# Optimization experiments

Measured on AMD Instinct MI355X. Metric: run time of the kernel, lower is better.

The kernel has to match this reference:

```python
import jax, jax.numpy as jnp
import numpy as np

D_MODEL = 1024
D_FF = 4096
LN_EPS = 1e-5


def _layer_norm(x, gamma, beta):
    mu = jnp.mean(x, axis=-1, keepdims=True)
    var = jnp.mean(jnp.square(x - mu), axis=-1, keepdims=True)
    return (x - mu) * jax.lax.rsqrt(var + LN_EPS) * gamma + beta


def setup_inputs() -> dict:
    key = jax.random.key(0)
    ks = jax.random.split(key, 16)
    B, S, D, F = 2, 2048, D_MODEL, D_FF
    s_d = 1.0 / np.sqrt(D)
    s_f = 1.0 / np.sqrt(F)
    u = lambda k, shape, s: jax.random.uniform(k, shape, jnp.float32, -s, s)
    return {
        "x": jax.random.normal(ks[0], (B, S, D), jnp.float32),
        "wq": u(ks[1], (D, D), s_d), "bq": u(ks[2], (D,), s_d),
        "wk": u(ks[3], (D, D), s_d), "bk": u(ks[4], (D,), s_d),
        "wv": u(ks[5], (D, D), s_d), "bv": u(ks[6], (D,), s_d),
        "wo": u(ks[7], (D, D), s_d), "bo": u(ks[8], (D,), s_d),
        "w1": u(ks[9], (F, D), s_d), "b1": u(ks[10], (F,), s_d),
        "w2": u(ks[11], (D, F), s_f), "b2": u(ks[12], (D,), s_f),
        "g1": jnp.ones((D,), jnp.float32), "be1": jnp.zeros((D,), jnp.float32),
        "g2": jnp.ones((D,), jnp.float32), "be2": jnp.zeros((D,), jnp.float32),
        "num_heads": 16,
    }


def reference(x, wq, bq, wk, bk, wv, bv, wo, bo, w1, b1, w2, b2, g1, be1, g2, be2, num_heads):
    B, S, D = x.shape
    H = num_heads
    dk = D // H
    scale = 1.0 / np.sqrt(dk)

    # --- self-attention (pre-norm) ---
    h = _layer_norm(x, g1, be1)
    q = (h @ wq.T + bq).reshape(B, S, H, dk)
    k = (h @ wk.T + bk).reshape(B, S, H, dk)
    v = (h @ wv.T + bv).reshape(B, S, H, dk)
    scores = jnp.einsum("bqhd,bkhd->bhqk", q, k) * scale  # [B,H,S,S]
    attn = jax.nn.softmax(scores, axis=-1)
    ctx = jnp.einsum("bhqk,bkhd->bqhd", attn, v).reshape(B, S, D)
    x = x + ctx @ wo.T + bo

    # --- feed-forward (pre-norm, exact GELU as in torch default) ---
    h = _layer_norm(x, g2, be2)
    h = jax.nn.gelu(h @ w1.T + b1, approximate=False)
    x = x + h @ w2.T + b2
    return x
```

## Files before the change

kernel.cpp:

```cpp
#include <hip/hip_runtime.h>

typedef __attribute__((ext_vector_type(8))) __bf16 bf16x8;
typedef __attribute__((ext_vector_type(4))) __bf16 bf16x4;
typedef __attribute__((ext_vector_type(4))) float floatx4;
typedef void __attribute__((address_space(3))) lds_void_t;
typedef const void __attribute__((address_space(1))) gbl_void_t;

#define D_MODEL 1024
#define SEQ     2048
#define BATCH   2
#define NH      16
#define DK      64
#define DFF     4096
#define NTOK    (BATCH * SEQ)
#define QKVS    3072

#if __has_builtin(__builtin_amdgcn_exp2f)
#define EXP2(x) __builtin_amdgcn_exp2f(x)
#else
#define EXP2(x) exp2f(x)
#endif

__device__ __forceinline__ float gelu_exact(float x) {
    return 0.5f * x * (1.0f + erff(x * 0.70710678118654752f));
}

__global__ __launch_bounds__(256) void cast_f32_bf16(const float* __restrict__ src,
                                                     __bf16* __restrict__ dst, int n) {
    int i = (blockIdx.x * 256 + threadIdx.x) * 8;
    if (i >= n) return;
    floatx4 a = *(const floatx4*)(src + i);
    floatx4 b = *(const floatx4*)(src + i + 4);
    bf16x8 o;
    for (int j = 0; j < 4; ++j) { o[j] = (__bf16)a[j]; o[4 + j] = (__bf16)b[j]; }
    *(bf16x8*)(dst + i) = o;
}

__global__ __launch_bounds__(64) void ln_kernel(const float* __restrict__ x,
                                                const float* __restrict__ g,
                                                const float* __restrict__ b,
                                                __bf16* __restrict__ out) {
    int row = blockIdx.x, lane = threadIdx.x, base = lane * 16;
    const float* xr = x + (size_t)row * D_MODEL + base;
    float v[16];
    for (int j = 0; j < 4; ++j) {
        floatx4 a = *(const floatx4*)(xr + 4 * j);
        for (int i = 0; i < 4; ++i) v[4 * j + i] = a[i];
    }
    float s = 0.f, sq = 0.f;
    for (int i = 0; i < 16; ++i) { s += v[i]; sq += v[i] * v[i]; }
    for (int o = 1; o < 64; o <<= 1) { s += __shfl_xor(s, o); sq += __shfl_xor(sq, o); }
    float mu = s * (1.0f / D_MODEL);
    float var = sq * (1.0f / D_MODEL) - mu * mu;
    float rstd = rsqrtf(fmaxf(var, 0.f) + 1e-5f);

    const floatx4* gp = (const floatx4*)(g + base);
    const floatx4* bp = (const floatx4*)(b + base);
    bf16x8 o0, o1;
    for (int j = 0; j < 2; ++j) {
        floatx4 gv0 = gp[2 * j], gv1 = gp[2 * j + 1];
        floatx4 bv0 = bp[2 * j], bv1 = bp[2 * j + 1];
        for (int i = 0; i < 4; ++i) {
            float r0 = (v[8 * j + i] - mu) * rstd * gv0[i] + bv0[i];
            float r1 = (v[8 * j + 4 + i] - mu) * rstd * gv1[i] + bv1[i];
            if (j == 0) { o0[i] = (__bf16)r0; o0[4 + i] = (__bf16)r1; }
            else        { o1[i] = (__bf16)r0; o1[4 + i] = (__bf16)r1; }
        }
    }
    bf16x8* op = (bf16x8*)(out + (size_t)row * D_MODEL + base);
    op[0] = o0; op[1] = o1;
}

template <typename OutT, bool GELU, bool TRIBIAS, int KSPLIT>
__global__ __launch_bounds__(256) void gemm_bt(const __bf16* __restrict__ A,
                                               const __bf16* __restrict__ W,
                                               const float* __restrict__ bias0,
                                               const float* __restrict__ bias1,
                                               const float* __restrict__ bias2,
                                               const float* __restrict__ res,
                                               OutT* out, float* part1,
                                               int M, int N, int K) {
    __shared__ __bf16 As[2][128][32];
    __shared__ __bf16 Ws[2][128][32];

    int m0 = blockIdx.y * 128, n0 = blockIdx.x * 128;
    int t = threadIdx.x;
    int lane = t & 63, wave = t >> 6;
    int wm = (wave >> 1) * 64, wn = (wave & 1) * 64;
    int fr = lane & 15, quad = lane >> 4;
    int srow = t >> 2, scol = (t & 3) * 8;

    int Ks = K / KSPLIT;
    int kbeg = (KSPLIT > 1) ? blockIdx.z * Ks : 0;

    floatx4 acc[4][4] = {};

    const __bf16* Ab = A + (size_t)(m0 + srow) * K + kbeg + scol;
    const __bf16* Wb = W + (size_t)(n0 + srow) * K + kbeg + scol;

    auto stage = [&](int buf, int k0) {
        __builtin_amdgcn_global_load_lds((gbl_void_t*)(Ab + k0),
                                         (lds_void_t*)&As[buf][wave * 16][0], 16, 0, 0);
        __builtin_amdgcn_global_load_lds((gbl_void_t*)(Ab + (size_t)64 * K + k0),
                                         (lds_void_t*)&As[buf][64 + wave * 16][0], 16, 0, 0);
        __builtin_amdgcn_global_load_lds((gbl_void_t*)(Wb + k0),
                                         (lds_void_t*)&Ws[buf][wave * 16][0], 16, 0, 0);
        __builtin_amdgcn_global_load_lds((gbl_void_t*)(Wb + (size_t)64 * K + k0),
                                         (lds_void_t*)&Ws[buf][64 + wave * 16][0], 16, 0, 0);
    };

    stage(0, 0);
    int nsteps = Ks / 32;
    for (int s = 0; s < nsteps; ++s) {
        int cur = s & 1;
        __syncthreads();
        if (s + 1 < nsteps) stage(cur ^ 1, (s + 1) * 32);

        bf16x8 af[4], wf[4];
#pragma unroll
        for (int i = 0; i < 4; ++i) af[i] = *(const bf16x8*)&As[cur][wm + i * 16 + fr][quad * 8];
#pragma unroll
        for (int i = 0; i < 4; ++i) wf[i] = *(const bf16x8*)&Ws[cur][wn + i * 16 + fr][quad * 8];
#pragma unroll
        for (int mi = 0; mi < 4; ++mi)
#pragma unroll
            for (int ni = 0; ni < 4; ++ni)
                acc[mi][ni] = __builtin_amdgcn_mfma_f32_16x16x32_bf16(af[mi], wf[ni], acc[mi][ni], 0, 0, 0);
    }

    if (KSPLIT > 1) {
        float* pb = (blockIdx.z == 0) ? (float*)out : part1;
#pragma unroll
        for (int ni = 0; ni < 4; ++ni) {
            int col = n0 + wn + ni * 16 + fr;
#pragma unroll
            for (int mi = 0; mi < 4; ++mi)
#pragma unroll
                for (int r = 0; r < 4; ++r) {
                    int row = m0 + wm + mi * 16 + quad * 4 + r;
                    pb[(size_t)row * N + col] = acc[mi][ni][r];
                }
        }
    } else {
#pragma unroll
        for (int ni = 0; ni < 4; ++ni) {
            int col = n0 + wn + ni * 16 + fr;
            const float* bp = bias0;
            int bcol = col;
            if (TRIBIAS) { bp = col < 1024 ? bias0 : (col < 2048 ? bias1 : bias2); bcol = col & 1023; }
            float bv = bp[bcol];
#pragma unroll
            for (int mi = 0; mi < 4; ++mi) {
#pragma unroll
                for (int r = 0; r < 4; ++r) {
                    int row = m0 + wm + mi * 16 + quad * 4 + r;
                    float v = acc[mi][ni][r] + bv;
                    if (GELU) v = gelu_exact(v);
                    if (res) v += res[(size_t)row * N + col];
                    out[(size_t)row * N + col] = (OutT)v;
                }
            }
        }
    }
}

__global__ __launch_bounds__(256) void reduce_k2(const float* __restrict__ p0,
                                                 const float* p1,
                                                 const float* __restrict__ res,
                                                 const float* __restrict__ bias,
                                                 float* out) {
    int i = (blockIdx.x * 256 + threadIdx.x) * 4;
    floatx4 a = *(const floatx4*)(p0 + i);
    floatx4 b = *(const floatx4*)(p1 + i);
    floatx4 r = *(const floatx4*)(res + i);
    floatx4 bv = *(const floatx4*)(bias + (i & 1023));
    floatx4 o;
#pragma unroll
    for (int j = 0; j < 4; ++j) o[j] = a[j] + b[j] + r[j] + bv[j];
    *(floatx4*)(out + i) = o;
}

__global__ __launch_bounds__(256) void transpose_v(const __bf16* __restrict__ qkv,
                                                   __bf16* __restrict__ vt) {
    __shared__ __bf16 tile[64][72];
    int b = blockIdx.z, h = blockIdx.y, s0 = blockIdx.x * 64;
    int t = threadIdx.x;
    int dl = (t & 7) * 8, sl = t >> 3;
    for (int p = 0; p < 2; ++p) {
        int s = sl + p * 32;
        bf16x8 val = *(const bf16x8*)(qkv + (size_t)(b * SEQ + s0 + s) * QKVS + 2048 + h * DK + dl);
        *(bf16x8*)&tile[s][dl] = val;
    }
    __syncthreads();
    int sl2 = (t & 7) * 8, d = t >> 3;
    for (int p = 0; p < 2; ++p) {
        int dd = d + p * 32;
        bf16x8 val;
        for (int j = 0; j < 8; ++j) val[j] = tile[sl2 + j][dd];
        *(bf16x8*)(vt + ((size_t)(b * NH + h) * DK + dd) * SEQ + s0 + sl2) = val;
    }
}

__global__ __launch_bounds__(256, 2) void attn_kernel(const __bf16* __restrict__ qkv,
                                                      const __bf16* __restrict__ vt,
                                                      __bf16* __restrict__ ctx) {
    __shared__ __bf16 Klds[8192];
    __shared__ __bf16 Vlds[8192];
    __shared__ __bf16 Plds[4][32][136];
    int b = blockIdx.z, h = blockIdx.y;
    int wave = threadIdx.x >> 6, lane = threadIdx.x & 63;
    int q0 = blockIdx.x * 128 + wave * 32;
    int fr = lane & 15, quad = lane >> 4;
    const float sc2 = 0.18033688011112042f;

    const __bf16* qp0 = qkv + (size_t)(b * SEQ + q0 + fr) * QKVS + h * DK + quad * 8;
    const __bf16* qp1 = qp0 + (size_t)16 * QKVS;
    bf16x8 qA0 = *(const bf16x8*)qp0, qB0 = *(const bf16x8*)(qp0 + 32);
    bf16x8 qA1 = *(const bf16x8*)qp1, qB1 = *(const bf16x8*)(qp1 + 32);

    const __bf16* kg = qkv + (size_t)b * SEQ * QKVS + 1024 + h * DK;
    const __bf16* vg = vt + (size_t)(b * NH + h) * DK * SEQ;

    floatx4 o[8] = {};
    float m0q = -1e30f, l0q = 0.f, m1q = -1e30f, l1q = 0.f;

    auto stage_tile = [&](int k0) {
#pragma unroll
        for (int p = 0; p < 4; ++p) {
            int bid = wave * 4 + p;
            int f = bid >> 1, half = bid & 1;
            __builtin_amdgcn_global_load_lds(
                (gbl_void_t*)(kg + (size_t)(k0 + f * 16 + fr) * QKVS + quad * 8 + half * 32),
                (lds_void_t*)&Klds[bid * 512], 16, 0, 0);
            int c = bid >> 2, ti = bid & 3;
            __builtin_amdgcn_global_load_lds(
                (gbl_void_t*)(vg + (size_t)(ti * 16 + fr) * SEQ + k0 + c * 32 + quad * 8),
                (lds_void_t*)&Vlds[bid * 512], 16, 0, 0);
        }
    };

    stage_tile(0);
    __syncthreads();

    for (int k0 = 0; k0 < SEQ; k0 += 128) {
        const __bf16* Kb = Klds + lane * 8;
        const __bf16* Vb = Vlds + lane * 8;
        bf16x8 kA[8], kB[8];
#pragma unroll
        for (int f = 0; f < 8; ++f) {
            kA[f] = *(const bf16x8*)(Kb + (f * 2 + 0) * 512);
            kB[f] = *(const bf16x8*)(Kb + (f * 2 + 1) * 512);
        }

        floatx4 s[8];
#pragma unroll
        for (int f = 0; f < 8; ++f) {
            floatx4 z = {0.f, 0.f, 0.f, 0.f};
            z = __builtin_amdgcn_mfma_f32_16x16x32_bf16(kA[f], qA0, z, 0, 0, 0);
            s[f] = __builtin_amdgcn_mfma_f32_16x16x32_bf16(kB[f], qB0, z, 0, 0, 0);
        }
        {
            float fm[8];
#pragma unroll
            for (int f = 0; f < 8; ++f)
                fm[f] = fmaxf(fmaxf(s[f][0], s[f][1]), fmaxf(s[f][2], s[f][3]));
            float mx = fmaxf(fmaxf(fmaxf(fm[0], fm[1]), fmaxf(fm[2], fm[3])),
                             fmaxf(fmaxf(fm[4], fm[5]), fmaxf(fm[6], fm[7])));
            float mx2 = mx * sc2;
            mx2 = fmaxf(mx2, __shfl_xor(mx2, 16));
            mx2 = fmaxf(mx2, __shfl_xor(mx2, 32));
            float mn = fmaxf(m0q, mx2);
            float alpha = EXP2(m0q - mn);
            m0q = mn;
            float r0 = 0.f, r1 = 0.f, r2 = 0.f, r3 = 0.f;
#pragma unroll
            for (int f = 0; f < 8; ++f) {
                bf16x4 pk;
                float p0 = EXP2(fmaf(s[f][0], sc2, -mn));
                float p1 = EXP2(fmaf(s[f][1], sc2, -mn));
                float p2 = EXP2(fmaf(s[f][2], sc2, -mn));
                float p3 = EXP2(fmaf(s[f][3], sc2, -mn));
                r0 += p0; r1 += p1; r2 += p2; r3 += p3;
                pk[0] = (__bf16)p0; pk[1] = (__bf16)p1; pk[2] = (__bf16)p2; pk[3] = (__bf16)p3;
                *(bf16x4*)&Plds[wave][fr][f * 16 + quad * 4] = pk;
            }
            float rs = (r0 + r1) + (r2 + r3);
            rs += __shfl_xor(rs, 16);
            rs += __shfl_xor(rs, 32);
            l0q = l0q * alpha + rs;
            float aB[4];
#pragma unroll
            for (int r = 0; r < 4; ++r) aB[r] = __shfl(alpha, quad * 4 + r);
#pragma unroll
            for (int ti = 0; ti < 4; ++ti)
#pragma unroll
                for (int r = 0; r < 4; ++r) o[ti][r] *= aB[r];
        }

        floatx4 s1[8];
#pragma unroll
        for (int f = 0; f < 8; ++f) {
            floatx4 z = {0.f, 0.f, 0.f, 0.f};
            z = __builtin_amdgcn_mfma_f32_16x16x32_bf16(kA[f], qA1, z, 0, 0, 0);
            s1[f] = __builtin_amdgcn_mfma_f32_16x16x32_bf16(kB[f], qB1, z, 0, 0, 0);
        }

        bf16x8 vf[4][4];
#pragma unroll
        for (int c = 0; c < 4; ++c)
#pragma unroll
            for (int ti = 0; ti < 4; ++ti)
                vf[c][ti] = *(const bf16x8*)(Vb + (c * 4 + ti) * 512);

        __syncthreads();
        if (k0 + 128 < SEQ) stage_tile(k0 + 128);

        {
            float fm[8];
#pragma unroll
            for (int f = 0; f < 8; ++f)
                fm[f] = fmaxf(fmaxf(s1[f][0], s1[f][1]), fmaxf(s1[f][2], s1[f][3]));
            float mx = fmaxf(fmaxf(fmaxf(fm[0], fm[1]), fmaxf(fm[2], fm[3])),
                             fmaxf(fmaxf(fm[4], fm[5]), fmaxf(fm[6], fm[7])));
            float mx2 = mx * sc2;
            mx2 = fmaxf(mx2, __shfl_xor(mx2, 16));
            mx2 = fmaxf(mx2, __shfl_xor(mx2, 32));
            float mn = fmaxf(m1q, mx2);
            float alpha = EXP2(m1q - mn);
            m1q = mn;
            float r0 = 0.f, r1 = 0.f, r2 = 0.f, r3 = 0.f;
#pragma unroll
            for (int f = 0; f < 8; ++f) {
                bf16x4 pk;
                float p0 = EXP2(fmaf(s1[f][0], sc2, -mn));
                float p1 = EXP2(fmaf(s1[f][1], sc2, -mn));
                float p2 = EXP2(fmaf(s1[f][2], sc2, -mn));
                float p3 = EXP2(fmaf(s1[f][3], sc2, -mn));
                r0 += p0; r1 += p1; r2 += p2; r3 += p3;
                pk[0] = (__bf16)p0; pk[1] = (__bf16)p1; pk[2] = (__bf16)p2; pk[3] = (__bf16)p3;
                *(bf16x4*)&Plds[wave][16 + fr][f * 16 + quad * 4] = pk;
            }
            float rs = (r0 + r1) + (r2 + r3);
            rs += __shfl_xor(rs, 16);
            rs += __shfl_xor(rs, 32);
            l1q = l1q * alpha + rs;
            float aB[4];
#pragma unroll
            for (int r = 0; r < 4; ++r) aB[r] = __shfl(alpha, quad * 4 + r);
#pragma unroll
            for (int ti = 0; ti < 4; ++ti)
#pragma unroll
                for (int r = 0; r < 4; ++r) o[4 + ti][r] *= aB[r];
        }
        __threadfence_block();

        bf16x8 pa0[4], pa1[4];
#pragma unroll
        for (int c = 0; c < 4; ++c) {
            pa0[c] = *(const bf16x8*)&Plds[wave][fr][c * 32 + quad * 8];
            pa1[c] = *(const bf16x8*)&Plds[wave][16 + fr][c * 32 + quad * 8];
        }
#pragma unroll
        for (int c = 0; c < 4; ++c)
#pragma unroll
            for (int ti = 0; ti < 4; ++ti) {
                o[ti]     = __builtin_amdgcn_mfma_f32_16x16x32_bf16(pa0[c], vf[c][ti], o[ti], 0, 0, 0);
                o[4 + ti] = __builtin_amdgcn_mfma_f32_16x16x32_bf16(pa1[c], vf[c][ti], o[4 + ti], 0, 0, 0);
            }
        __threadfence_block();

        __syncthreads();
    }
    float lB0[4], lB1[4];
#pragma unroll
    for (int r = 0; r < 4; ++r) {
        lB0[r] = __shfl(l0q, quad * 4 + r);
        lB1[r] = __shfl(l1q, quad * 4 + r);
    }
#pragma unroll
    for (int ti = 0; ti < 4; ++ti)
#pragma unroll
        for (int r = 0; r < 4; ++r) {
            ctx[(size_t)(b * SEQ + q0 + quad * 4 + r) * D_MODEL + h * DK + ti * 16 + fr] =
                (__bf16)(o[ti][r] / lB0[r]);
            ctx[(size_t)(b * SEQ + q0 + 16 + quad * 4 + r) * D_MODEL + h * DK + ti * 16 + fr] =
                (__bf16)(o[4 + ti][r] / lB1[r]);
        }
}

extern "C" void kernel_launch(void* const* d_in, const int* in_sizes, int n_in,
                              void* d_out, int out_size, void* d_ws, size_t ws_size,
                              hipStream_t stream) {
    const float* x   = (const float*)d_in[0];
    const float* wq  = (const float*)d_in[1];
    const float* bq  = (const float*)d_in[2];
    const float* wk  = (const float*)d_in[3];
    const float* bk  = (const float*)d_in[4];
    const float* wv  = (const float*)d_in[5];
    const float* bv  = (const float*)d_in[6];
    const float* wo  = (const float*)d_in[7];
    const float* bo  = (const float*)d_in[8];
    const float* w1  = (const float*)d_in[9];
    const float* b1  = (const float*)d_in[10];
    const float* w2  = (const float*)d_in[11];
    const float* b2  = (const float*)d_in[12];
    const float* g1  = (const float*)d_in[13];
    const float* be1 = (const float*)d_in[14];
    const float* g2  = (const float*)d_in[15];
    const float* be2 = (const float*)d_in[16];
    float* out = (float*)d_out;

    char* ws = (char*)d_ws;
    const size_t MB = 1024 * 1024;
    __bf16* wqkvB = (__bf16*)(ws);
    __bf16* woB   = (__bf16*)(ws + 6 * MB);
    __bf16* w1B   = (__bf16*)(ws + 8 * MB);
    __bf16* w2B   = (__bf16*)(ws + 16 * MB);
    __bf16* h1    = (__bf16*)(ws + 24 * MB);
    float*  x1    = (float*)(ws + 24 * MB);
    __bf16* qkv   = (__bf16*)(ws + 40 * MB);
    __bf16* vt    = (__bf16*)(ws + 64 * MB);
    __bf16* ffh   = (__bf16*)(ws + 40 * MB);
    float*  pA0   = (float*)(ws + 40 * MB);
    float*  pA1   = (float*)(ws + 56 * MB);
    float*  pF0   = (float*)(ws);
    __bf16* ctx   = (__bf16*)d_out;
    __bf16* h2    = (__bf16*)d_out;

    const int NDD = D_MODEL * D_MODEL;
    const int NDF = D_MODEL * DFF;
    cast_f32_bf16<<<NDD / 2048, 256, 0, stream>>>(wq, wqkvB, NDD);
    cast_f32_bf16<<<NDD / 2048, 256, 0, stream>>>(wk, wqkvB + NDD, NDD);
    cast_f32_bf16<<<NDD / 2048, 256, 0, stream>>>(wv, wqkvB + 2 * NDD, NDD);
    cast_f32_bf16<<<NDD / 2048, 256, 0, stream>>>(wo, woB, NDD);
    cast_f32_bf16<<<NDF / 2048, 256, 0, stream>>>(w1, w1B, NDF);
    cast_f32_bf16<<<NDF / 2048, 256, 0, stream>>>(w2, w2B, NDF);

    dim3 gQKV(QKVS / 128, NTOK / 128);
    dim3 gDz(D_MODEL / 128, NTOK / 128, 2);
    dim3 gF(DFF / 128, NTOK / 128);
    dim3 gTr(SEQ / 64, NH, BATCH);
    dim3 gAttn(SEQ / 128, NH, BATCH);
    int gRed = NTOK * D_MODEL / (256 * 4);

    ln_kernel<<<NTOK, 64, 0, stream>>>(x, g1, be1, h1);
    gemm_bt<__bf16, false, true, 1><<<gQKV, 256, 0, stream>>>(h1, wqkvB, bq, bk, bv, nullptr, qkv, nullptr, NTOK, QKVS, D_MODEL);
    transpose_v<<<gTr, 256, 0, stream>>>(qkv, vt);
    attn_kernel<<<gAttn, 256, 0, stream>>>(qkv, vt, ctx);
    gemm_bt<float, false, false, 2><<<gDz, 256, 0, stream>>>(ctx, woB, nullptr, nullptr, nullptr, nullptr, pA0, pA1, NTOK, D_MODEL, D_MODEL);
    reduce_k2<<<gRed, 256, 0, stream>>>(pA0, pA1, x, bo, x1);
    ln_kernel<<<NTOK, 64, 0, stream>>>(x1, g2, be2, h2);
    gemm_bt<__bf16, true, false, 1><<<gF, 256, 0, stream>>>(h2, w1B, b1, b1, b1, nullptr, ffh, nullptr, NTOK, DFF, D_MODEL);
    gemm_bt<float, false, false, 2><<<gDz, 256, 0, stream>>>(ffh, w2B, nullptr, nullptr, nullptr, nullptr, pF0, (float*)d_out, NTOK, D_MODEL, DFF);
    reduce_k2<<<gRed, 256, 0, stream>>>(pF0, (float*)d_out, x1, b2, out);
}
```

Before: 417.7 us.

## Triple-buffer GEMM LDS tiles with fragment-ordered layout and partial vmcnt waits

Replaces the double-buffered GEMM mainloop with a three-stage LDS ring that keeps two K-tiles in flight, using explicit s_waitcnt vmcnt(4) and raw barriers instead of __syncthreads. The LDS tiles are also stored in MFMA fragment order so each lane reads a contiguous 16-byte chunk, which removes strided LDS reads and bank conflicts. The goal is to hide global load latency behind MFMA work. The cost is more LDS per block, which may lower occupancy, and fragile hand-set wait counts.

```diff
diff --git a/kernel.cpp b/kernel.cpp
--- a/kernel.cpp
+++ b/kernel.cpp
@@ -80,53 +80,72 @@
                                                const float* __restrict__ res,
                                                OutT* out, float* part1,
                                                int M, int N, int K) {
-    __shared__ __bf16 As[2][128][32];
-    __shared__ __bf16 Ws[2][128][32];
+    __shared__ __bf16 AsF[3][4096];
+    __shared__ __bf16 WsF[3][4096];
 
     int m0 = blockIdx.y * 128, n0 = blockIdx.x * 128;
     int t = threadIdx.x;
     int lane = t & 63, wave = t >> 6;
     int wm = (wave >> 1) * 64, wn = (wave & 1) * 64;
     int fr = lane & 15, quad = lane >> 4;
-    int srow = t >> 2, scol = (t & 3) * 8;
+    int scol = quad * 8;
 
     int Ks = K / KSPLIT;
     int kbeg = (KSPLIT > 1) ? blockIdx.z * Ks : 0;
 
     floatx4 acc[4][4] = {};
 
-    const __bf16* Ab = A + (size_t)(m0 + srow) * K + kbeg + scol;
-    const __bf16* Wb = W + (size_t)(n0 + srow) * K + kbeg + scol;
+    const __bf16* Abase = A + kbeg;
+    const __bf16* Wbase = W + kbeg;
 
     auto stage = [&](int buf, int k0) {
-        __builtin_amdgcn_global_load_lds((gbl_void_t*)(Ab + k0),
-                                         (lds_void_t*)&As[buf][wave * 16][0], 16, 0, 0);
-        __builtin_amdgcn_global_load_lds((gbl_void_t*)(Ab + (size_t)64 * K + k0),
-                                         (lds_void_t*)&As[buf][64 + wave * 16][0], 16, 0, 0);
-        __builtin_amdgcn_global_load_lds((gbl_void_t*)(Wb + k0),
-                                         (lds_void_t*)&Ws[buf][wave * 16][0], 16, 0, 0);
-        __builtin_amdgcn_global_load_lds((gbl_void_t*)(Wb + (size_t)64 * K + k0),
-                                         (lds_void_t*)&Ws[buf][64 + wave * 16][0], 16, 0, 0);
+#pragma unroll
+        for (int p = 0; p < 2; ++p) {
+            int blk = p * 4 + wave;
+            int row = (blk >> 2) * 64 + (blk & 3) * 16 + fr;
+            __builtin_amdgcn_global_load_lds(
+                (gbl_void_t*)(Abase + (size_t)(m0 + row) * K + k0 + scol),
+                (lds_void_t*)&AsF[buf][blk * 512], 16, 0, 0);
+            __builtin_amdgcn_global_load_lds(
+                (gbl_void_t*)(Wbase + (size_t)(n0 + row) * K + k0 + scol),
+                (lds_void_t*)&WsF[buf][blk * 512], 16, 0, 0);
+        }
     };
 
-    stage(0, 0);
-    int nsteps = Ks / 32;
-    for (int s = 0; s < nsteps; ++s) {
-        int cur = s & 1;
-        __syncthreads();
-        if (s + 1 < nsteps) stage(cur ^ 1, (s + 1) * 32);
-
+    auto compute = [&](int buf) {
         bf16x8 af[4], wf[4];
 #pragma unroll
-        for (int i = 0; i < 4; ++i) af[i] = *(const bf16x8*)&As[cur][wm + i * 16 + fr][quad * 8];
-#pragma unroll
-        for (int i = 0; i < 4; ++i) wf[i] = *(const bf16x8*)&Ws[cur][wn + i * 16 + fr][quad * 8];
+        for (int i = 0; i < 4; ++i)
+            af[i] = *(const bf16x8*)&AsF[buf][((wave >> 1) * 4 + i) * 512 + lane * 8];
+#pragma unroll
+        for (int i = 0; i < 4; ++i)
+            wf[i] = *(const bf16x8*)&WsF[buf][((wave & 1) * 4 + i) * 512 + lane * 8];
 #pragma unroll
         for (int mi = 0; mi < 4; ++mi)
 #pragma unroll
             for (int ni = 0; ni < 4; ++ni)
                 acc[mi][ni] = __builtin_amdgcn_mfma_f32_16x16x32_bf16(af[mi], wf[ni], acc[mi][ni], 0, 0, 0);
-    }
+    };
+
+    int nsteps = Ks / 32;
+    stage(0, 0);
+    stage(1, 32);
+    int cur = 0;
+    for (int s = 0; s < nsteps - 1; ++s) {
+        asm volatile("s_waitcnt vmcnt(4)" ::: "memory");
+        __builtin_amdgcn_s_barrier();
+        __builtin_amdgcn_sched_barrier(0);
+        if (s + 2 < nsteps) {
+            int b2 = cur + 2; if (b2 >= 3) b2 -= 3;
+            stage(b2, (s + 2) * 32);
+        }
+        compute(cur);
+        cur = (cur == 2) ? 0 : cur + 1;
+    }
+    asm volatile("s_waitcnt vmcnt(0)" ::: "memory");
+    __builtin_amdgcn_s_barrier();
+    __builtin_amdgcn_sched_barrier(0);
+    compute(cur);
 
     if (KSPLIT > 1) {
         float* pb = (blockIdx.z == 0) ? (float*)out : part1;
```

Result: slower. 474.4 us (+13.6%).
